# Kernel tuning notes

Hardware: AMD Instinct MI355X
Metric: run time of the kernel (lower is better)

Reference implementation:

```python
import jax, jax.numpy as jnp
import numpy as np

D_MODEL = 768
N_HEADS = 12
HEAD_DIM = D_MODEL // N_HEADS


def setup_inputs() -> dict:
    key = jax.random.key(0)
    ks = jax.random.split(key, 9)
    s = 1.0 / np.sqrt(D_MODEL)
    inp = {
        "inputs": jax.random.normal(ks[0], (1, 4096, D_MODEL), dtype=jnp.float32),
        "Wq": jax.random.uniform(ks[1], (D_MODEL, D_MODEL), jnp.float32, -s, s),
        "bq": jax.random.uniform(ks[2], (D_MODEL,), jnp.float32, -s, s),
        "Wk": jax.random.uniform(ks[3], (D_MODEL, D_MODEL), jnp.float32, -s, s),
        "bk": jax.random.uniform(ks[4], (D_MODEL,), jnp.float32, -s, s),
        "Wv": jax.random.uniform(ks[5], (D_MODEL, D_MODEL), jnp.float32, -s, s),
        "bv": jax.random.uniform(ks[6], (D_MODEL,), jnp.float32, -s, s),
        "Wo": jax.random.uniform(ks[7], (D_MODEL, D_MODEL), jnp.float32, -s, s),
        "bo": jax.random.uniform(ks[8], (D_MODEL,), jnp.float32, -s, s),
    }
    return inp


def reference(inputs, Wq, bq, Wk, bk, Wv, bv, Wo, bo):
    B, S, D = inputs.shape
    H, Hd = N_HEADS, HEAD_DIM

    def split_heads(x):  # [B,S,D] -> [B,H,S,Hd]
        return x.reshape(B, S, H, Hd).transpose(0, 2, 1, 3)

    # nn.Linear computes x @ W.T + b
    Q = split_heads(inputs @ Wq.T + bq)
    K = split_heads(inputs @ Wk.T + bk)
    V = split_heads(inputs @ Wv.T + bv)

    scores = jnp.einsum("bhsd,bhtd->bhst", Q, K) / jnp.sqrt(jnp.float32(Hd))
    causal = jnp.tril(jnp.ones((S, S), dtype=bool))  # True = keep
    scores = jnp.where(causal, scores, -jnp.inf)
    attn = jax.nn.softmax(scores, axis=-1)  # dropout is identity in eval

    out = jnp.einsum("bhst,bhtd->bhsd", attn, V)
    out = out.transpose(0, 2, 1, 3).reshape(B, S, D)
    return out @ Wo.T + bo
```

## Files before the change

kernel.cpp:

```cpp
#include <hip/hip_runtime.h>
#include <stdint.h>

#define SEQ 4096
#define DM 768
#define NH 12
#define HD 64

typedef unsigned short u16;
typedef short short8 __attribute__((ext_vector_type(8)));
typedef float floatx4 __attribute__((ext_vector_type(4)));
typedef float floatx16 __attribute__((ext_vector_type(16)));
typedef u16 u16x4 __attribute__((ext_vector_type(4)));

__device__ inline u16 f2b(float f) {
  union { float f; uint32_t u; } v; v.f = f;
  uint32_t u = v.u;
  return (u16)((u + 0x7fffu + ((u >> 16) & 1u)) >> 16);
}

__device__ inline float b2f(u16 x) {
  union { uint32_t u; float f; } v; v.u = ((uint32_t)x) << 16;
  return v.f;
}

#if defined(__has_builtin)
#if __has_builtin(__builtin_amdgcn_cvt_pk_bf16_f32)
#define HAVE_PK_BF16 1
#endif
#endif

__device__ inline uint32_t pk_bf16(float a, float b) {
#ifdef HAVE_PK_BF16
  typedef __bf16 bf16x2_t __attribute__((ext_vector_type(2)));
  union { bf16x2_t v; uint32_t u; } c;
  c.v = __builtin_amdgcn_cvt_pk_bf16_f32(a, b);
  return c.u;
#else
  uint32_t r;
  asm("v_cvt_pk_bf16_f32 %0, %1, %2" : "=v"(r) : "v"(a), "v"(b));
  return r;
#endif
}

__device__ inline void pl32swap(uint32_t& a, uint32_t& b) {
  asm("v_permlane32_swap_b32 %0, %1" : "+v"(a), "+v"(b));
}

__device__ inline void load_lds16(const void* g, void* l) {
  __builtin_amdgcn_global_load_lds(
      (const __attribute__((address_space(1))) uint32_t*)g,
      (__attribute__((address_space(3))) uint32_t*)l, 16, 0, 0);
}

__global__ __launch_bounds__(256) void convert_all(
    const float* __restrict__ X, const float* __restrict__ Wq,
    const float* __restrict__ Wk, const float* __restrict__ Wv,
    const float* __restrict__ Wo,
    u16* __restrict__ Xb, u16* __restrict__ Wqb, u16* __restrict__ Wkb,
    u16* __restrict__ Wvb, u16* __restrict__ Wob) {
  int t = blockIdx.x * 256 + threadIdx.x;
  const int NX = SEQ * DM / 4;
  const int NW = DM * DM / 4;
  const float* src; u16* dst; int off;
  if (t < NX)               { src = X;  dst = Xb;  off = t; }
  else if (t < NX + NW)     { src = Wq; dst = Wqb; off = t - NX; }
  else if (t < NX + 2 * NW) { src = Wk; dst = Wkb; off = t - NX - NW; }
  else if (t < NX + 3 * NW) { src = Wv; dst = Wvb; off = t - NX - 2 * NW; }
  else if (t < NX + 4 * NW) { src = Wo; dst = Wob; off = t - NX - 3 * NW; }
  else return;
  float4 v = *(const float4*)(src + (size_t)off * 4);
  uint2 o;
  o.x = pk_bf16(v.x, v.y);
  o.y = pk_bf16(v.z, v.w);
  *(uint2*)(dst + (size_t)off * 4) = o;
}

__global__ __launch_bounds__(256) void gemm_qkv(
    const u16* __restrict__ Xb,
    const u16* __restrict__ Wqb, const u16* __restrict__ Wkb,
    const u16* __restrict__ Wvb,
    const float* __restrict__ bq, const float* __restrict__ bk,
    const float* __restrict__ bv,
    u16* __restrict__ Qh, u16* __restrict__ Kh, u16* __restrict__ VtG) {
  const u16* W; const float* bias;
  const int z = blockIdx.z;
  if (z == 0)      { W = Wqb; bias = bq; }
  else if (z == 1) { W = Wkb; bias = bk; }
  else             { W = Wvb; bias = bv; }

  __shared__ u16 smem[16384];

  const int tid = threadIdx.x;
  const int wave = tid >> 6, lane = tid & 63;
  const int g = lane >> 4, ln = lane & 15;
  const int m0 = blockIdx.y * 64, n0 = blockIdx.x * 64;
  const int wm = (wave & 1) * 32, wn = (wave >> 1) * 32;
  const int srow = lane >> 3;
  const int schunk = (lane & 7) ^ srow;
  const int swz = ln & 7;

  floatx4 acc[2][2] = {};

#pragma unroll
  for (int i = 0; i < 2; ++i) {
    int u = wave * 2 + i;
    load_lds16(Xb + (size_t)(m0 + u * 8 + srow) * DM + schunk * 8, smem + u * 512);
    load_lds16(W + (size_t)(n0 + u * 8 + srow) * DM + schunk * 8,
               smem + 8192 + u * 512);
  }

  for (int kt = 0; kt < 12; ++kt) {
    const int cur = kt & 1;
    __syncthreads();
    if (kt < 11) {
      const int k0 = (kt + 1) * 64, nb = cur ^ 1;
#pragma unroll
      for (int i = 0; i < 2; ++i) {
        int u = wave * 2 + i;
        load_lds16(Xb + (size_t)(m0 + u * 8 + srow) * DM + k0 + schunk * 8,
                   smem + nb * 4096 + u * 512);
        load_lds16(W + (size_t)(n0 + u * 8 + srow) * DM + k0 + schunk * 8,
                   smem + 8192 + nb * 4096 + u * 512);
      }
    }
    const u16* Ac = smem + cur * 4096;
    const u16* Bc = smem + 8192 + cur * 4096;
    short8 af[2][2], bf[2][2];
#pragma unroll
    for (int mi = 0; mi < 2; ++mi)
#pragma unroll
      for (int kh = 0; kh < 2; ++kh)
        af[mi][kh] = *(const short8*)(Ac + (wm + mi * 16 + ln) * 64 +
                                      ((kh * 4 + g) ^ swz) * 8);
#pragma unroll
    for (int ni = 0; ni < 2; ++ni)
#pragma unroll
      for (int kh = 0; kh < 2; ++kh)
        bf[ni][kh] = *(const short8*)(Bc + (wn + ni * 16 + ln) * 64 +
                                      ((kh * 4 + g) ^ swz) * 8);
#pragma unroll
    for (int kh = 0; kh < 2; ++kh)
#pragma unroll
      for (int mi = 0; mi < 2; ++mi)
#pragma unroll
        for (int ni = 0; ni < 2; ++ni)
          acc[mi][ni] = __builtin_amdgcn_mfma_f32_16x16x32_bf16(
              af[mi][kh], bf[ni][kh], acc[mi][ni], 0, 0, 0);
  }

  const float qscale = 0.125f * 1.44269504089f;
  const int hh = n0 >> 6;
  __syncthreads();

  if (z == 2) {
#pragma unroll
    for (int mi = 0; mi < 2; ++mi) {
      int row0 = wm + mi * 16 + g * 4;
#pragma unroll
      for (int ni = 0; ni < 2; ++ni) {
        int col = wn + ni * 16 + ln;
        float b = bias[n0 + col];
        uint2 o;
        o.x = pk_bf16(acc[mi][ni][0] + b, acc[mi][ni][1] + b);
        o.y = pk_bf16(acc[mi][ni][2] + b, acc[mi][ni][3] + b);
        *(uint2*)(smem + col * 72 + row0) = o;
      }
    }
    __syncthreads();
#pragma unroll
    for (int t = 0; t < 2; ++t) {
      int unit = tid + t * 256;
      int dcol = unit >> 3, ch = unit & 7;
      short8 v = *(const short8*)(smem + dcol * 72 + ch * 8);
      *(short8*)(VtG + ((size_t)(hh * 64 + dcol)) * SEQ + m0 + ch * 8) = v;
    }
  } else {
    u16* out = (z == 0) ? Qh : Kh;
    float cs = (z == 0) ? qscale : 1.0f;
#pragma unroll
    for (int mi = 0; mi < 2; ++mi) {
      int row0 = wm + mi * 16 + g * 4;
#pragma unroll
      for (int ni = 0; ni < 2; ++ni) {
        int col = wn + ni * 16 + ln;
        float b = bias[n0 + col];
        uint32_t w0 = pk_bf16((acc[mi][ni][0] + b) * cs, (acc[mi][ni][1] + b) * cs);
        uint32_t w1 = pk_bf16((acc[mi][ni][2] + b) * cs, (acc[mi][ni][3] + b) * cs);
        smem[(row0 + 0) * 72 + col] = (u16)w0;
        smem[(row0 + 1) * 72 + col] = (u16)(w0 >> 16);
        smem[(row0 + 2) * 72 + col] = (u16)w1;
        smem[(row0 + 3) * 72 + col] = (u16)(w1 >> 16);
      }
    }
    __syncthreads();
#pragma unroll
    for (int t = 0; t < 2; ++t) {
      int unit = tid + t * 256;
      int row = unit >> 3, ch = unit & 7;
      short8 v = *(const short8*)(smem + row * 72 + ch * 8);
      *(short8*)(out + ((size_t)hh * SEQ + m0 + row) * HD + ch * 8) = v;
    }
  }
}

#define CHUNK 16
#define M0 40.0f
__global__ __launch_bounds__(256, 4) void attn_chunk(
    const u16* __restrict__ Qh, const u16* __restrict__ Kh,
    const u16* __restrict__ VtG, u16* __restrict__ Opart,
    float2* __restrict__ Mlp) {
  const int h = blockIdx.x;
  const int b = 79 - blockIdx.y;
  int qB, ci;
  if (b < 8)       { qB = b;               ci = 0; }
  else if (b < 24) { int r = b - 8;  qB = 8 + (r >> 1); ci = r & 1; }
  else if (b < 48) { int r = b - 24; int d = r / 3; qB = 16 + d; ci = r - d * 3; }
  else             { int r = b - 48; qB = 24 + (r >> 2); ci = r & 3; }
  const int kb0 = ci * CHUNK;
  const int kb1 = min(kb0 + CHUNK, 2 * qB + 2);

  const int tid = threadIdx.x, wave = tid >> 6, lane = tid & 63;
  const int hi = lane >> 5, lq = lane & 31;
  const int q0 = qB * 128;
  const int qwave = q0 + wave * 32;
  const int srow = lane >> 3;
  const int schunk = (lane & 7) ^ srow;
  const int rsw = lane & 7;

  __shared__ u16 Ks[2 * 4096];
  __shared__ u16 Vt[2 * 4096];

  const int qglob = qwave + lq;
  const u16* Qbase = Qh + ((size_t)h * SEQ + qglob) * HD;
  short8 aq[4];
#pragma unroll
  for (int s = 0; s < 4; ++s)
    aq[s] = *(const short8*)(Qbase + s * 16 + hi * 8);

  floatx16 oacc[2] = {};
  floatx4 lacc = {};

  const size_t kbase = (size_t)h * SEQ * HD;
  const size_t vbase = (size_t)h * 64 * SEQ;

#pragma unroll
  for (int i = 0; i < 2; ++i) {
    int u = wave * 2 + i;
    load_lds16(Kh + kbase + (size_t)(kb0 * 64 + u * 8 + srow) * HD + schunk * 8,
               Ks + u * 512);
    load_lds16(VtG + vbase + (size_t)(u * 8 + srow) * SEQ + kb0 * 64 + schunk * 8,
               Vt + u * 512);
  }

  for (int kb = kb0; kb < kb1; ++kb) {
    const int cur = (kb - kb0) & 1;
    __syncthreads();
    if (kb + 1 < kb1) {
      const int nb = cur ^ 1, kn = (kb + 1) * 64;
#pragma unroll
      for (int i = 0; i < 2; ++i) {
        int u = wave * 2 + i;
        load_lds16(Kh + kbase + (size_t)(kn + u * 8 + srow) * HD + schunk * 8,
                   Ks + nb * 4096 + u * 512);
        load_lds16(VtG + vbase + (size_t)(u * 8 + srow) * SEQ + kn + schunk * 8,
                   Vt + nb * 4096 + u * 512);
      }
    }
    const u16* Kc = Ks + cur * 4096;
    const u16* Vc = Vt + cur * 4096;

    if (kb * 64 > qwave + 31) continue;

    floatx16 st[2];
#pragma unroll
    for (int kblk = 0; kblk < 2; ++kblk)
#pragma unroll
      for (int r = 0; r < 16; ++r) st[kblk][r] = -M0;
    __builtin_amdgcn_s_setprio(1);
#pragma unroll
    for (int s = 0; s < 4; ++s)
#pragma unroll
      for (int kblk = 0; kblk < 2; ++kblk) {
        short8 kf = *(const short8*)(Kc + (kblk * 32 + lq) * 64 +
                                     ((s * 2 + hi) ^ rsw) * 8);
        st[kblk] = __builtin_amdgcn_mfma_f32_32x32x16_bf16(kf, aq[s], st[kblk],
                                                           0, 0, 0);
      }
    __builtin_amdgcn_s_setprio(0);

    if (kb * 64 + 63 > qwave) {
#pragma unroll
      for (int kblk = 0; kblk < 2; ++kblk)
#pragma unroll
        for (int r = 0; r < 16; ++r) {
          int key = kb * 64 + kblk * 32 + (r & 3) + 8 * (r >> 2) + 4 * hi;
          if (key > qglob) st[kblk][r] = -1e30f;
        }
    }

    uint32_t w[2][8];
#pragma unroll
    for (int kblk = 0; kblk < 2; ++kblk) {
#pragma unroll
      for (int r = 0; r < 16; ++r)
        st[kblk][r] = __builtin_amdgcn_exp2f(st[kblk][r]);
#pragma unroll
      for (int r = 0; r < 4; ++r)
        lacc[r] += st[kblk][r] + st[kblk][4 + r] + st[kblk][8 + r] +
                   st[kblk][12 + r];
#pragma unroll
      for (int i = 0; i < 8; ++i)
        w[kblk][i] = pk_bf16(st[kblk][2 * i], st[kblk][2 * i + 1]);
    }

    __builtin_amdgcn_s_setprio(1);
#pragma unroll
    for (int ks = 0; ks < 4; ++ks) {
      const int kblk = ks >> 1, base = (ks & 1) * 4;
      uint32_t d0 = w[kblk][base + 0], d2 = w[kblk][base + 2];
      uint32_t d1 = w[kblk][base + 1], d3 = w[kblk][base + 3];
      pl32swap(d0, d2);
      pl32swap(d1, d3);
      union { uint32_t u[4]; short8 s; } bp;
      bp.u[0] = d0; bp.u[1] = d1; bp.u[2] = d2; bp.u[3] = d3;
#pragma unroll
      for (int dblk = 0; dblk < 2; ++dblk) {
        short8 vf = *(const short8*)(Vc + (dblk * 32 + lq) * 64 +
                                     ((ks * 2 + hi) ^ rsw) * 8);
        oacc[dblk] = __builtin_amdgcn_mfma_f32_32x32x16_bf16(vf, bp.s, oacc[dblk],
                                                             0, 0, 0);
      }
    }
    __builtin_amdgcn_s_setprio(0);
  }

  float l_i = lacc[0] + lacc[1] + lacc[2] + lacc[3];
  l_i += __shfl_xor(l_i, 32);

  const int slot = (h * 32 + qB) * 4 + ci;
  float inv = 1.f / l_i;
  int qloc = wave * 32 + lq;
  u16* Op = Opart + (size_t)slot * 8192 + qloc * 64;
#pragma unroll
  for (int dblk = 0; dblk < 2; ++dblk)
#pragma unroll
    for (int qd = 0; qd < 4; ++qd) {
      uint2 o;
      o.x = pk_bf16(oacc[dblk][qd * 4 + 0] * inv, oacc[dblk][qd * 4 + 1] * inv);
      o.y = pk_bf16(oacc[dblk][qd * 4 + 2] * inv, oacc[dblk][qd * 4 + 3] * inv);
      *(uint2*)(Op + dblk * 32 + qd * 8 + hi * 4) = o;
    }
  if (hi == 0) Mlp[(size_t)slot * 128 + qloc] = make_float2(M0, l_i);
}

__global__ __launch_bounds__(256) void attn_merge(
    const u16* __restrict__ Opart, const float2* __restrict__ Mlp,
    u16* __restrict__ Ob) {
  const int h = blockIdx.x, qB = blockIdx.y;
  const int n = (qB >> 3) + 1;
  const int base = (h * 32 + qB) * 4;
  const int q = threadIdx.x >> 1;
  const int d0 = (threadIdx.x & 1) * 32;

  float m[4], l[4];
  float M = -1e30f;
  for (int i = 0; i < n; ++i) {
    float2 ml = Mlp[(size_t)(base + i) * 128 + q];
    m[i] = ml.x; l[i] = ml.y;
    M = fmaxf(M, m[i]);
  }
  float w[4], L = 0.f;
  for (int i = 0; i < n; ++i) {
    w[i] = l[i] * __builtin_amdgcn_exp2f(m[i] - M);
    L += w[i];
  }
  float invL = 1.f / L;

  float acc[32];
#pragma unroll
  for (int j = 0; j < 32; ++j) acc[j] = 0.f;
  for (int i = 0; i < n; ++i) {
    float wi = w[i] * invL;
    const u16* src = Opart + (size_t)(base + i) * 8192 + q * 64 + d0;
#pragma unroll
    for (int c = 0; c < 4; ++c) {
      short8 a = ((const short8*)src)[c];
#pragma unroll
      for (int j = 0; j < 8; ++j) acc[c * 8 + j] += wi * b2f((u16)a[j]);
    }
  }

  u16* dst = Ob + (size_t)(qB * 128 + q) * DM + h * HD + d0;
#pragma unroll
  for (int c = 0; c < 4; ++c) {
    uint4 o;
    o.x = pk_bf16(acc[c * 8 + 0], acc[c * 8 + 1]);
    o.y = pk_bf16(acc[c * 8 + 2], acc[c * 8 + 3]);
    o.z = pk_bf16(acc[c * 8 + 4], acc[c * 8 + 5]);
    o.w = pk_bf16(acc[c * 8 + 6], acc[c * 8 + 7]);
    ((uint4*)dst)[c] = o;
  }
}

__global__ __launch_bounds__(256) void gemm_out(
    const u16* __restrict__ Ab, const u16* __restrict__ Wob,
    const float* __restrict__ bo, float* __restrict__ Cout) {
  __shared__ u16 smem[16384];

  const int tid = threadIdx.x;
  const int wave = tid >> 6, lane = tid & 63;
  const int g = lane >> 4, ln = lane & 15;
  const int m0 = blockIdx.y * 64, n0 = blockIdx.x * 64;
  const int wm = (wave & 1) * 32, wn = (wave >> 1) * 32;
  const int srow = lane >> 3;
  const int schunk = (lane & 7) ^ srow;
  const int swz = ln & 7;

  floatx4 acc[2][2] = {};

#pragma unroll
  for (int i = 0; i < 2; ++i) {
    int u = wave * 2 + i;
    load_lds16(Ab + (size_t)(m0 + u * 8 + srow) * DM + schunk * 8, smem + u * 512);
    load_lds16(Wob + (size_t)(n0 + u * 8 + srow) * DM + schunk * 8,
               smem + 8192 + u * 512);
  }

  for (int kt = 0; kt < 12; ++kt) {
    const int cur = kt & 1;
    __syncthreads();
    if (kt < 11) {
      const int k0 = (kt + 1) * 64, nb = cur ^ 1;
#pragma unroll
      for (int i = 0; i < 2; ++i) {
        int u = wave * 2 + i;
        load_lds16(Ab + (size_t)(m0 + u * 8 + srow) * DM + k0 + schunk * 8,
                   smem + nb * 4096 + u * 512);
        load_lds16(Wob + (size_t)(n0 + u * 8 + srow) * DM + k0 + schunk * 8,
                   smem + 8192 + nb * 4096 + u * 512);
      }
    }
    const u16* Ac = smem + cur * 4096;
    const u16* Bc = smem + 8192 + cur * 4096;
    short8 af[2][2], bf[2][2];
#pragma unroll
    for (int mi = 0; mi < 2; ++mi)
#pragma unroll
      for (int kh = 0; kh < 2; ++kh)
        af[mi][kh] = *(const short8*)(Ac + (wm + mi * 16 + ln) * 64 +
                                      ((kh * 4 + g) ^ swz) * 8);
#pragma unroll
    for (int ni = 0; ni < 2; ++ni)
#pragma unroll
      for (int kh = 0; kh < 2; ++kh)
        bf[ni][kh] = *(const short8*)(Bc + (wn + ni * 16 + ln) * 64 +
                                      ((kh * 4 + g) ^ swz) * 8);
#pragma unroll
    for (int kh = 0; kh < 2; ++kh)
#pragma unroll
      for (int mi = 0; mi < 2; ++mi)
#pragma unroll
        for (int ni = 0; ni < 2; ++ni)
          acc[mi][ni] = __builtin_amdgcn_mfma_f32_16x16x32_bf16(
              af[mi][kh], bf[ni][kh], acc[mi][ni], 0, 0, 0);
  }

#pragma unroll
  for (int mi = 0; mi < 2; ++mi) {
    int row = m0 + wm + mi * 16 + g * 4;
#pragma unroll
    for (int ni = 0; ni < 2; ++ni) {
      int col = n0 + wn + ni * 16 + ln;
      float b = bo[col];
#pragma unroll
      for (int r = 0; r < 4; ++r)
        Cout[(size_t)(row + r) * DM + col] = acc[mi][ni][r] + b;
    }
  }
}

extern "C" void kernel_launch(void* const* d_in, const int* in_sizes, int n_in,
                              void* d_out, int out_size, void* d_ws, size_t ws_size,
                              hipStream_t stream) {
  const float* X  = (const float*)d_in[0];
  const float* Wq = (const float*)d_in[1];
  const float* bq = (const float*)d_in[2];
  const float* Wk = (const float*)d_in[3];
  const float* bk = (const float*)d_in[4];
  const float* Wv = (const float*)d_in[5];
  const float* bv = (const float*)d_in[6];
  const float* Wo = (const float*)d_in[7];
  const float* bo = (const float*)d_in[8];
  float* out = (float*)d_out;

  char* ws = (char*)d_ws;
  u16* Xb  = (u16*)ws; ws += (size_t)SEQ * DM * 2;
  u16* Wqb = (u16*)ws; ws += (size_t)DM * DM * 2;
  u16* Wkb = (u16*)ws; ws += (size_t)DM * DM * 2;
  u16* Wvb = (u16*)ws; ws += (size_t)DM * DM * 2;
  u16* Wob = (u16*)ws; ws += (size_t)DM * DM * 2;
  u16* Qh  = (u16*)ws; ws += (size_t)NH * SEQ * HD * 2;
  u16* Kh  = (u16*)ws; ws += (size_t)NH * SEQ * HD * 2;
  u16* VtG = (u16*)ws; ws += (size_t)NH * SEQ * HD * 2;
  u16* Ob  = (u16*)ws; ws += (size_t)SEQ * DM * 2;
  u16* Opart = (u16*)ws; ws += (size_t)NH * 32 * 4 * 128 * 64 * 2;
  float2* Mlp = (float2*)ws; ws += (size_t)NH * 32 * 4 * 128 * sizeof(float2);

  convert_all<<<5376, 256, 0, stream>>>(X, Wq, Wk, Wv, Wo, Xb, Wqb, Wkb, Wvb, Wob);

  dim3 gq(DM / 64, SEQ / 64, 3);
  gemm_qkv<<<gq, 256, 0, stream>>>(Xb, Wqb, Wkb, Wvb, bq, bk, bv, Qh, Kh, VtG);

  dim3 ga(NH, 80);
  attn_chunk<<<ga, 256, 0, stream>>>(Qh, Kh, VtG, Opart, Mlp);

  dim3 gm(NH, 32);
  attn_merge<<<gm, 256, 0, stream>>>(Opart, Mlp, Ob);

  dim3 go(DM / 64, SEQ / 64);
  gemm_out<<<go, 256, 0, stream>>>(Ob, Wob, bo, out);
}
```

Before: 171.3 us.

## Triple-buffer K/V tiles with vmcnt waits and remap block order

The attention chunk kernel moves from double to triple buffering of K/V tiles in LDS. It now prefetches two tiles ahead and uses explicit s_waitcnt vmcnt plus s_barrier in place of __syncthreads, so global loads have more time to land before they are consumed. It also remaps the block index so head/query-block work is interleaved across the 24-slot dispatch cycle, and it lowers launch bounds occupancy from 4 to 3 to fit the larger LDS footprint. The risks are lower occupancy and the correctness of hand-written wait counts (vmcnt(4) assumes four loads per stage).

Result: slower. 176.9 us (+3.2%).

```diff
diff --git a/kernel.cpp b/kernel.cpp
--- a/kernel.cpp
+++ b/kernel.cpp
@@ -205,12 +205,15 @@
 
 #define CHUNK 16
 #define M0 40.0f
-__global__ __launch_bounds__(256, 4) void attn_chunk(
+__global__ __launch_bounds__(256, 3) void attn_chunk(
     const u16* __restrict__ Qh, const u16* __restrict__ Kh,
     const u16* __restrict__ VtG, u16* __restrict__ Opart,
     float2* __restrict__ Mlp) {
-  const int h = blockIdx.x;
-  const int b = 79 - blockIdx.y;
+  const int p = blockIdx.y * NH + blockIdx.x;
+  const int slot = p % 24, cyc = p / 24;
+  const int qq = 3 * (slot & 7) + (slot >> 3);
+  const int h = qq >> 1;
+  const int b = 79 - (cyc * 2 + (qq & 1));
   int qB, ci;
   if (b < 8)       { qB = b;               ci = 0; }
   else if (b < 24) { int r = b - 8;  qB = 8 + (r >> 1); ci = r & 1; }
@@ -227,8 +230,8 @@
   const int schunk = (lane & 7) ^ srow;
   const int rsw = lane & 7;
 
-  __shared__ u16 Ks[2 * 4096];
-  __shared__ u16 Vt[2 * 4096];
+  __shared__ u16 Ks[3 * 4096];
+  __shared__ u16 Vt[3 * 4096];
 
   const int qglob = qwave + lq;
   const u16* Qbase = Qh + ((size_t)h * SEQ + qglob) * HD;
@@ -243,29 +246,27 @@
   const size_t kbase = (size_t)h * SEQ * HD;
   const size_t vbase = (size_t)h * 64 * SEQ;
 
-#pragma unroll
-  for (int i = 0; i < 2; ++i) {
-    int u = wave * 2 + i;
-    load_lds16(Kh + kbase + (size_t)(kb0 * 64 + u * 8 + srow) * HD + schunk * 8,
-               Ks + u * 512);
-    load_lds16(VtG + vbase + (size_t)(u * 8 + srow) * SEQ + kb0 * 64 + schunk * 8,
-               Vt + u * 512);
-  }
+  auto stage = [&](int kbIdx, int buf) {
+#pragma unroll
+    for (int i = 0; i < 2; ++i) {
+      int u = wave * 2 + i;
+      load_lds16(Kh + kbase + (size_t)(kbIdx * 64 + u * 8 + srow) * HD + schunk * 8,
+                 Ks + buf * 4096 + u * 512);
+      load_lds16(VtG + vbase + (size_t)(u * 8 + srow) * SEQ + kbIdx * 64 + schunk * 8,
+                 Vt + buf * 4096 + u * 512);
+    }
+  };
+
+  stage(kb0, 0);
+  if (kb0 + 1 < kb1) stage(kb0 + 1, 1);
 
   for (int kb = kb0; kb < kb1; ++kb) {
-    const int cur = (kb - kb0) & 1;
-    __syncthreads();
-    if (kb + 1 < kb1) {
-      const int nb = cur ^ 1, kn = (kb + 1) * 64;
-#pragma unroll
-      for (int i = 0; i < 2; ++i) {
-        int u = wave * 2 + i;
-        load_lds16(Kh + kbase + (size_t)(kn + u * 8 + srow) * HD + schunk * 8,
-                   Ks + nb * 4096 + u * 512);
-        load_lds16(VtG + vbase + (size_t)(u * 8 + srow) * SEQ + kn + schunk * 8,
-                   Vt + nb * 4096 + u * 512);
-      }
-    }
+    const int cur = (kb - kb0) % 3;
+    if (kb + 1 < kb1) asm volatile("s_waitcnt vmcnt(4)" ::: "memory");
+    else              asm volatile("s_waitcnt vmcnt(0)" ::: "memory");
+    __builtin_amdgcn_s_barrier();
+    if (kb + 2 < kb1) stage(kb + 2, (cur + 2) % 3);
+
     const u16* Kc = Ks + cur * 4096;
     const u16* Vc = Vt + cur * 4096;
 
@@ -337,10 +338,10 @@
   float l_i = lacc[0] + lacc[1] + lacc[2] + lacc[3];
   l_i += __shfl_xor(l_i, 32);
 
-  const int slot = (h * 32 + qB) * 4 + ci;
+  const int slot2 = (h * 32 + qB) * 4 + ci;
   float inv = 1.f / l_i;
   int qloc = wave * 32 + lq;
-  u16* Op = Opart + (size_t)slot * 8192 + qloc * 64;
+  u16* Op = Opart + (size_t)slot2 * 8192 + qloc * 64;
 #pragma unroll
   for (int dblk = 0; dblk < 2; ++dblk)
 #pragma unroll
@@ -350,7 +351,7 @@
       o.y = pk_bf16(oacc[dblk][qd * 4 + 2] * inv, oacc[dblk][qd * 4 + 3] * inv);
       *(uint2*)(Op + dblk * 32 + qd * 8 + hi * 4) = o;
     }
-  if (hi == 0) Mlp[(size_t)slot * 128 + qloc] = make_float2(M0, l_i);
+  if (hi == 0) Mlp[(size_t)slot2 * 128 + qloc] = make_float2(M0, l_i);
 }
 
 __global__ __launch_bounds__(256) void attn_merge(
```
